# Kernel optimization log

Measured on AMD Instinct MI355X. Metric: run time of the kernel, lower is better.

## Reference

```python
import jax, jax.numpy as jnp
import numpy as np

N_NODES = 40000
N_EDGES = 640000
D = 128
D_OUT = 128


def setup_inputs() -> dict:
    key = jax.random.key(0)
    k1, k2, k3, k4, k5 = jax.random.split(key, 5)
    x = jax.random.normal(k1, (N_NODES, D), dtype=jnp.float32)
    edge_index = jax.random.randint(k2, (2, N_EDGES), 0, N_NODES, dtype=jnp.int64)
    edge_weight = jax.random.uniform(k3, (N_EDGES,), dtype=jnp.float32)
    W = jax.random.normal(k4, (D_OUT, 2 * D), dtype=jnp.float32) / np.sqrt(2 * D)
    b = jax.random.normal(k5, (D_OUT,), dtype=jnp.float32) * 0.01
    return {"x": x, "edge_index": edge_index, "edge_weight": edge_weight, "W": W, "b": b}


def reference(x, edge_index, edge_weight, W, b):
    src, dst = edge_index[0], edge_index[1]
    n_dst = x.shape[0]
    # gather source features per edge: [E, D]
    msgs = x[src]
    # per-destination weight sums (degree-normalization denominator)
    w_sum = jax.ops.segment_sum(edge_weight, dst, num_segments=n_dst)
    w_norm = edge_weight / jnp.clip(w_sum[dst], 1e-8, None)
    # weighted scatter-add aggregation: [N, D]
    agg = jax.ops.segment_sum(w_norm[:, None] * msgs, dst, num_segments=n_dst)
    # concat self + aggregated neighbors, project
    h = jnp.concatenate([x, agg], axis=-1)
    return h @ W.T + b
```

## Files before the change

### kernel.cpp

```cpp
#include <hip/hip_runtime.h>

constexpr int NN = 40000;
constexpr int NE = 640000;
constexpr int NBKT = 625;

typedef __attribute__((ext_vector_type(8))) short short8;
typedef __attribute__((ext_vector_type(4))) float f32x4;

__device__ __forceinline__ unsigned short rneb(float f) {
    unsigned u = __float_as_uint(f);
    u = (u + 0x7FFFu + ((u >> 16) & 1u)) >> 16;
    return (unsigned short)u;
}
__device__ __forceinline__ float b2f(unsigned short s) {
    return __uint_as_float(((unsigned)s) << 16);
}

__global__ void zero_k(int* __restrict__ g) {
    int t = threadIdx.x;
    if (t < NBKT) g[t] = 0;
}

__global__ __launch_bounds__(256) void cvtx_k(const float* __restrict__ x,
                                              unsigned short* __restrict__ xb) {
    int g = blockIdx.x * 256 + threadIdx.x;
    float4 v = reinterpret_cast<const float4*>(x)[g];
    ushort4 o = { rneb(v.x), rneb(v.y), rneb(v.z), rneb(v.w) };
    reinterpret_cast<ushort4*>(xb)[g] = o;
}

__global__ void cvtw_k(const float* __restrict__ W, unsigned short* __restrict__ Wb) {
    int g = blockIdx.x * 256 + threadIdx.x;
    if (g >= 128 * 64) return;
    float4 v = reinterpret_cast<const float4*>(W)[g];
    ushort4 o = { rneb(v.x), rneb(v.y), rneb(v.z), rneb(v.w) };
    reinterpret_cast<ushort4*>(Wb)[g] = o;
}

__global__ __launch_bounds__(1024) void ccount_k(const int* __restrict__ dst,
                                                 int* __restrict__ gcnt) {
    __shared__ int cnt[NBKT];
    int t = threadIdx.x;
    if (t < NBKT) cnt[t] = 0;
    __syncthreads();
    int eb = blockIdx.x * 5000;
    for (int i = t; i < 5000; i += 1024)
        atomicAdd(&cnt[dst[eb + i] >> 6], 1);
    __syncthreads();
    if (t < NBKT && cnt[t]) atomicAdd(&gcnt[t], cnt[t]);
}

__global__ __launch_bounds__(1024) void cscan_k(const int* __restrict__ gcnt,
                                                int* __restrict__ bptr,
                                                int* __restrict__ cursor) {
    __shared__ int sc[1024];
    int t = threadIdx.x;
    int c = (t < NBKT) ? gcnt[t] : 0;
    sc[t] = c;
    __syncthreads();
    for (int o = 1; o < 1024; o <<= 1) {
        int u = (t >= o) ? sc[t - o] : 0;
        __syncthreads();
        sc[t] += u;
        __syncthreads();
    }
    if (t < NBKT) {
        int excl = sc[t] - c;
        bptr[t]   = excl;
        cursor[t] = excl;
    }
    if (t == 0) bptr[NBKT] = NE;
}

__global__ __launch_bounds__(1024) void cscatter_k(const int* __restrict__ dst,
                                                   const int* __restrict__ src,
                                                   const float* __restrict__ ew,
                                                   int* __restrict__ cursor,
                                                   unsigned* __restrict__ rec,
                                                   unsigned char* __restrict__ dloc) {
    __shared__ int cnt[NBKT];
    __shared__ int base[NBKT];
    int t = threadIdx.x;
    if (t < NBKT) cnt[t] = 0;
    __syncthreads();
    int eb = blockIdx.x * 5000;
    for (int i = t; i < 5000; i += 1024)
        atomicAdd(&cnt[dst[eb + i] >> 6], 1);
    __syncthreads();
    if (t < NBKT) {
        base[t] = atomicAdd(&cursor[t], cnt[t]);
        cnt[t]  = 0;
    }
    __syncthreads();
    for (int i = t; i < 5000; i += 1024) {
        int d   = dst[eb + i];
        int bkt = d >> 6;
        int slot = atomicAdd(&cnt[bkt], 1);
        int p = base[bkt] + slot;
        unsigned short wh = __builtin_bit_cast(unsigned short, (_Float16)ew[eb + i]);
        rec[p]  = (unsigned)src[eb + i] | ((unsigned)wh << 16);
        dloc[p] = (unsigned char)(d & 63);
    }
}

__global__ __launch_bounds__(1024) void agg3_k(const unsigned* __restrict__ rec,
                                               const unsigned char* __restrict__ dloc,
                                               const int* __restrict__ bptr,
                                               const unsigned short* __restrict__ xb,
                                               float* __restrict__ out) {
    constexpr int CAP = 2048;
    __shared__ unsigned grec[CAP];
    __shared__ int cnt[64];
    __shared__ int cur[64];
    __shared__ int pL[65];
    int bkt = blockIdx.x, t = threadIdx.x;
    int beg = bptr[bkt], end = bptr[bkt + 1];
    int grp = t >> 4, fl = t & 15;
    float acc[8] = {0.f, 0.f, 0.f, 0.f, 0.f, 0.f, 0.f, 0.f};
    float wsv = 0.f;

    for (int cb = beg; cb < end; cb += CAP) {
        int m = end - cb; if (m > CAP) m = CAP;
        if (t < 64) cnt[t] = 0;
        __syncthreads();
        unsigned r0 = 0, r1 = 0; int d0 = -1, d1 = -1;
        if (t < m)        { r0 = rec[cb + t];        d0 = dloc[cb + t];        atomicAdd(&cnt[d0], 1); }
        if (t + 1024 < m) { r1 = rec[cb + t + 1024]; d1 = dloc[cb + t + 1024]; atomicAdd(&cnt[d1], 1); }
        __syncthreads();
        if (t < 64) {
            int v = cnt[t], s = v;
            #pragma unroll
            for (int o = 1; o < 64; o <<= 1) {
                int u = __shfl_up(s, o);
                if (t >= o) s += u;
            }
            pL[t]  = s - v;
            cur[t] = s - v;
            if (t == 63) pL[64] = s;
        }
        __syncthreads();
        if (d0 >= 0) { int p = atomicAdd(&cur[d0], 1); grec[p] = r0; }
        if (d1 >= 0) { int p = atomicAdd(&cur[d1], 1); grec[p] = r1; }
        __syncthreads();
        int gb = pL[grp], ge = pL[grp + 1];
        for (int e = gb; e < ge; ++e) {
            unsigned r = grec[e];
            int s = r & 0xFFFF;
            float w = (float)__builtin_bit_cast(_Float16, (unsigned short)(r >> 16));
            short8 v = *reinterpret_cast<const short8*>(xb + (size_t)s * 128 + fl * 8);
            wsv += w;
            #pragma unroll
            for (int i = 0; i < 8; ++i) acc[i] += w * b2f((unsigned short)v[i]);
        }
        __syncthreads();
    }

    int n = bkt * 64 + grp;
    float inv = 1.f / fmaxf(wsv, 1e-8f);
    float4 o0 = { acc[0] * inv, acc[1] * inv, acc[2] * inv, acc[3] * inv };
    float4 o1 = { acc[4] * inv, acc[5] * inv, acc[6] * inv, acc[7] * inv };
    float4* op = reinterpret_cast<float4*>(out + (size_t)n * 128 + fl * 8);
    op[0] = o0;
    op[1] = o1;
}

__global__ __launch_bounds__(256) void gemm_mfma_k(const unsigned short* __restrict__ xb,
                                                   const unsigned short* __restrict__ Wb,
                                                   const float* __restrict__ bias_p,
                                                   float* out) {
    int w = threadIdx.x >> 6, l = threadIdx.x & 63;
    int l15 = l & 15, lg = l >> 4;
    int rb = blockIdx.x * 128 + w * 32;

    f32x4 acc[2][8];
    #pragma unroll
    for (int i = 0; i < 2; ++i)
        #pragma unroll
        for (int c = 0; c < 8; ++c) acc[i][c] = (f32x4)0.f;

    float bias[8];
    #pragma unroll
    for (int c = 0; c < 8; ++c) bias[c] = bias_p[c * 16 + l15];

    int r0 = rb + l15;      if (r0 > NN - 1) r0 = NN - 1;
    int r1 = rb + 16 + l15; if (r1 > NN - 1) r1 = NN - 1;

    #pragma unroll
    for (int step = 0; step < 8; ++step) {
        int kg = step * 32 + lg * 8;
        short8 a0, a1;
        if (step < 4) {
            a0 = *reinterpret_cast<const short8*>(xb + (size_t)r0 * 128 + kg);
            a1 = *reinterpret_cast<const short8*>(xb + (size_t)r1 * 128 + kg);
        } else {
            const float* p0 = out + (size_t)r0 * 128 + (kg - 128);
            const float* p1 = out + (size_t)r1 * 128 + (kg - 128);
            float4 u0 = *reinterpret_cast<const float4*>(p0);
            float4 u1 = *reinterpret_cast<const float4*>(p0 + 4);
            float4 v0 = *reinterpret_cast<const float4*>(p1);
            float4 v1 = *reinterpret_cast<const float4*>(p1 + 4);
            a0 = short8{ (short)rneb(u0.x), (short)rneb(u0.y), (short)rneb(u0.z), (short)rneb(u0.w),
                         (short)rneb(u1.x), (short)rneb(u1.y), (short)rneb(u1.z), (short)rneb(u1.w) };
            a1 = short8{ (short)rneb(v0.x), (short)rneb(v0.y), (short)rneb(v0.z), (short)rneb(v0.w),
                         (short)rneb(v1.x), (short)rneb(v1.y), (short)rneb(v1.z), (short)rneb(v1.w) };
        }
        #pragma unroll
        for (int c = 0; c < 8; ++c) {
            short8 bf = *reinterpret_cast<const short8*>(Wb + (size_t)(c * 16 + l15) * 256 + kg);
            acc[0][c] = __builtin_amdgcn_mfma_f32_16x16x32_bf16(a0, bf, acc[0][c], 0, 0, 0);
            acc[1][c] = __builtin_amdgcn_mfma_f32_16x16x32_bf16(a1, bf, acc[1][c], 0, 0, 0);
        }
    }

    #pragma unroll
    for (int i = 0; i < 2; ++i) {
        int rbase = rb + i * 16 + lg * 4;
        #pragma unroll
        for (int c = 0; c < 8; ++c) {
            #pragma unroll
            for (int r = 0; r < 4; ++r) {
                int row = rbase + r;
                if (row < NN)
                    out[(size_t)row * 128 + c * 16 + l15] = acc[i][c][r] + bias[c];
            }
        }
    }
}


__global__ void wsum_k(const int* __restrict__ dst, const float* __restrict__ ew,
                       float* __restrict__ wsum) {
    int e = blockIdx.x * 256 + threadIdx.x;
    if (e < NE) atomicAdd(&wsum[dst[e]], ew[e]);
}

__global__ void zerof_k(float* __restrict__ p, int n4) {
    int g = blockIdx.x * 256 + threadIdx.x;
    if (g < n4) reinterpret_cast<float4*>(p)[g] = make_float4(0.f, 0.f, 0.f, 0.f);
}

__global__ void scatter_k(const int* __restrict__ src, const int* __restrict__ dst,
                          const float* __restrict__ ew, const float* __restrict__ wsum,
                          const float* __restrict__ x, float* __restrict__ agg) {
    int tid = blockIdx.x * 256 + threadIdx.x;
    int e = tid >> 5;
    int p = tid & 31;
    if (e >= NE) return;
    int s = src[e], dn = dst[e];
    float wn = ew[e] / fmaxf(wsum[dn], 1e-8f);
    float4 v = *reinterpret_cast<const float4*>(x + (size_t)s * 128 + p * 4);
    float* o = agg + (size_t)dn * 128 + p * 4;
    atomicAdd(o + 0, wn * v.x);
    atomicAdd(o + 1, wn * v.y);
    atomicAdd(o + 2, wn * v.z);
    atomicAdd(o + 3, wn * v.w);
}

__global__ __launch_bounds__(256) void gemm_f32_k(const float* __restrict__ x,
                                                  const float* __restrict__ agg,
                                                  const float* __restrict__ W,
                                                  const float* __restrict__ b,
                                                  float* __restrict__ out) {
    __shared__ float4 Wl[128 * 64];
    __shared__ float4 hl[16 * 64];
    int t = threadIdx.x;
    int base = blockIdx.x * 80;
    const float4* Wg = reinterpret_cast<const float4*>(W);
    #pragma unroll
    for (int i = 0; i < 32; ++i) {
        int f = t + i * 256;
        int r = f >> 6, kk = f & 63;
        Wl[r * 64 + (kk ^ (r & 7))] = Wg[f];
    }
    int jj = t & 63, wsl = t >> 6, sw = jj & 7;
    float bv[2] = { b[jj], b[jj + 64] };
    const float4* xg = reinterpret_cast<const float4*>(x);
    const float4* ag = reinterpret_cast<const float4*>(agg);
    for (int g = 0; g < 5; ++g) {
        int nbase = base + g * 16;
        __syncthreads();
        #pragma unroll
        for (int i = 0; i < 4; ++i) {
            int f = t + i * 256;
            int ln = f >> 6, kk = f & 63;
            size_t node = (size_t)(nbase + ln);
            hl[ln * 64 + kk] = (kk < 32) ? xg[node * 32 + kk] : ag[node * 32 + (kk - 32)];
        }
        __syncthreads();
        float acc[2][4];
        #pragma unroll
        for (int q = 0; q < 2; ++q)
            #pragma unroll
            for (int n = 0; n < 4; ++n) acc[q][n] = 0.f;
        #pragma unroll 4
        for (int kk = 0; kk < 64; ++kk) {
            float4 h[4];
            #pragma unroll
            for (int n = 0; n < 4; ++n) h[n] = hl[(wsl + 4 * n) * 64 + kk];
            #pragma unroll
            for (int q = 0; q < 2; ++q) {
                float4 wv = Wl[(jj + q * 64) * 64 + (kk ^ sw)];
                #pragma unroll
                for (int n = 0; n < 4; ++n)
                    acc[q][n] += wv.x * h[n].x + wv.y * h[n].y + wv.z * h[n].z + wv.w * h[n].w;
            }
        }
        #pragma unroll
        for (int q = 0; q < 2; ++q)
            #pragma unroll
            for (int n = 0; n < 4; ++n)
                out[(size_t)(nbase + wsl + 4 * n) * 128 + jj + q * 64] = acc[q][n] + bv[q];
    }
}

extern "C" void kernel_launch(void* const* d_in, const int* in_sizes, int n_in,
                              void* d_out, int out_size, void* d_ws, size_t ws_size,
                              hipStream_t stream) {
    const float* x  = (const float*)d_in[0];
    const int*   ei = (const int*)d_in[1];
    const float* ew = (const float*)d_in[2];
    const float* W  = (const float*)d_in[3];
    const float* b  = (const float*)d_in[4];
    float* out = (float*)d_out;
    const int* src = ei;
    const int* dst = ei + NE;

    const size_t off_cursor = 4096;
    const size_t off_gcnt   = 8192;
    const size_t off_Wb     = 16384;
    const size_t off_dloc   = 81920;
    const size_t off_rec    = 724992;
    const size_t off_xb     = 3284992;
    const size_t need = off_xb + (size_t)NN * 128 * 2;

    if (ws_size >= need) {
        int* bptr   = (int*)d_ws;
        int* cursor = (int*)((char*)d_ws + off_cursor);
        int* gcnt   = (int*)((char*)d_ws + off_gcnt);
        unsigned short* Wb = (unsigned short*)((char*)d_ws + off_Wb);
        unsigned char* dloc = (unsigned char*)((char*)d_ws + off_dloc);
        unsigned* rec = (unsigned*)((char*)d_ws + off_rec);
        unsigned short* xb = (unsigned short*)((char*)d_ws + off_xb);

        zero_k    <<<1, 1024, 0, stream>>>(gcnt);
        cvtx_k    <<<5000, 256, 0, stream>>>(x, xb);
        ccount_k  <<<128, 1024, 0, stream>>>(dst, gcnt);
        cscan_k   <<<1, 1024, 0, stream>>>(gcnt, bptr, cursor);
        cscatter_k<<<128, 1024, 0, stream>>>(dst, src, ew, cursor, rec, dloc);
        cvtw_k    <<<32, 256, 0, stream>>>(W, Wb);
        agg3_k    <<<NBKT, 1024, 0, stream>>>(rec, dloc, bptr, xb, out);
        gemm_mfma_k<<<(NN + 127) / 128, 256, 0, stream>>>(xb, Wb, b, out);
    } else {
        float* wsum = (float*)d_ws;
        float* agg  = out;
        zerof_k  <<<(NN / 4 + 255) / 256, 256, 0, stream>>>(wsum, NN / 4);
        zerof_k  <<<(NN * 32 + 255) / 256, 256, 0, stream>>>(agg, NN * 32);
        wsum_k   <<<(NE + 255) / 256, 256, 0, stream>>>(dst, ew, wsum);
        scatter_k<<<NE * 32 / 256, 256, 0, stream>>>(src, dst, ew, wsum, x, agg);
        gemm_f32_k<<<500, 256, 0, stream>>>(x, agg, W, b, out);
    }
}
```

Before: 97.04 us.

## Fuse aggregation with MFMA projection and merge prep kernels into one launch

Merges the x/W bf16 conversions and the bucket counting into a single prep kernel that writes per-block counts, which removes the zeroing kernel and the global atomics. Cscan now sums the per-block counts itself. The aggregation kernel keeps its normalized neighbor sums as bf16 in a swizzled shared-memory tile and runs the 64x128 output projection with MFMA in the same block. This avoids writing fp32 agg to out and reading it back in a separate GEMM, and cuts the launch count from eight to four. In exchange, 16 waves per block each compute only a small GEMM tile, re-reading W from global memory, and shared memory per block grows.

```diff
diff --git a/kernel.cpp b/kernel.cpp
--- a/kernel.cpp
+++ b/kernel.cpp
@@ -3,6 +3,7 @@
 constexpr int NN = 40000;
 constexpr int NE = 640000;
 constexpr int NBKT = 625;
+constexpr int CBLK = 128;
 
 typedef __attribute__((ext_vector_type(8))) short short8;
 typedef __attribute__((ext_vector_type(4))) float f32x4;
@@ -16,46 +17,44 @@
     return __uint_as_float(((unsigned)s) << 16);
 }
 
-__global__ void zero_k(int* __restrict__ g) {
-    int t = threadIdx.x;
-    if (t < NBKT) g[t] = 0;
-}
-
-__global__ __launch_bounds__(256) void cvtx_k(const float* __restrict__ x,
-                                              unsigned short* __restrict__ xb) {
-    int g = blockIdx.x * 256 + threadIdx.x;
-    float4 v = reinterpret_cast<const float4*>(x)[g];
-    ushort4 o = { rneb(v.x), rneb(v.y), rneb(v.z), rneb(v.w) };
-    reinterpret_cast<ushort4*>(xb)[g] = o;
-}
-
-__global__ void cvtw_k(const float* __restrict__ W, unsigned short* __restrict__ Wb) {
-    int g = blockIdx.x * 256 + threadIdx.x;
-    if (g >= 128 * 64) return;
-    float4 v = reinterpret_cast<const float4*>(W)[g];
-    ushort4 o = { rneb(v.x), rneb(v.y), rneb(v.z), rneb(v.w) };
-    reinterpret_cast<ushort4*>(Wb)[g] = o;
-}
-
-__global__ __launch_bounds__(1024) void ccount_k(const int* __restrict__ dst,
-                                                 int* __restrict__ gcnt) {
+__global__ __launch_bounds__(1024) void prep_k(const float* __restrict__ x,
+                                               unsigned short* __restrict__ xb,
+                                               const float* __restrict__ W,
+                                               unsigned short* __restrict__ Wb,
+                                               const int* __restrict__ dst,
+                                               int* __restrict__ gcnt2) {
     __shared__ int cnt[NBKT];
-    int t = threadIdx.x;
-    if (t < NBKT) cnt[t] = 0;
-    __syncthreads();
-    int eb = blockIdx.x * 5000;
-    for (int i = t; i < 5000; i += 1024)
-        atomicAdd(&cnt[dst[eb + i] >> 6], 1);
-    __syncthreads();
-    if (t < NBKT && cnt[t]) atomicAdd(&gcnt[t], cnt[t]);
-}
-
-__global__ __launch_bounds__(1024) void cscan_k(const int* __restrict__ gcnt,
+    int bid = blockIdx.x, t = threadIdx.x;
+    if (bid < 1250) {
+        int g = bid * 1024 + t;
+        float4 v = reinterpret_cast<const float4*>(x)[g];
+        ushort4 o = { rneb(v.x), rneb(v.y), rneb(v.z), rneb(v.w) };
+        reinterpret_cast<ushort4*>(xb)[g] = o;
+    } else if (bid < 1258) {
+        int g = (bid - 1250) * 1024 + t;
+        float4 v = reinterpret_cast<const float4*>(W)[g];
+        ushort4 o = { rneb(v.x), rneb(v.y), rneb(v.z), rneb(v.w) };
+        reinterpret_cast<ushort4*>(Wb)[g] = o;
+    } else {
+        int cb = bid - 1258;
+        if (t < NBKT) cnt[t] = 0;
+        __syncthreads();
+        int eb = cb * 5000;
+        for (int i = t; i < 5000; i += 1024)
+            atomicAdd(&cnt[dst[eb + i] >> 6], 1);
+        __syncthreads();
+        if (t < NBKT) gcnt2[cb * 640 + t] = cnt[t];
+    }
+}
+
+__global__ __launch_bounds__(1024) void cscan_k(const int* __restrict__ gcnt2,
                                                 int* __restrict__ bptr,
                                                 int* __restrict__ cursor) {
     __shared__ int sc[1024];
     int t = threadIdx.x;
-    int c = (t < NBKT) ? gcnt[t] : 0;
+    int c = 0;
+    if (t < NBKT)
+        for (int b = 0; b < CBLK; ++b) c += gcnt2[b * 640 + t];
     sc[t] = c;
     __syncthreads();
     for (int o = 1; o < 1024; o <<= 1) {
@@ -103,16 +102,19 @@
     }
 }
 
-__global__ __launch_bounds__(1024) void agg3_k(const unsigned* __restrict__ rec,
-                                               const unsigned char* __restrict__ dloc,
-                                               const int* __restrict__ bptr,
-                                               const unsigned short* __restrict__ xb,
-                                               float* __restrict__ out) {
+__global__ __launch_bounds__(1024) void aggemm_k(const unsigned* __restrict__ rec,
+                                                 const unsigned char* __restrict__ dloc,
+                                                 const int* __restrict__ bptr,
+                                                 const unsigned short* __restrict__ xb,
+                                                 const unsigned short* __restrict__ Wb,
+                                                 const float* __restrict__ bias_p,
+                                                 float* __restrict__ out) {
     constexpr int CAP = 2048;
     __shared__ unsigned grec[CAP];
     __shared__ int cnt[64];
     __shared__ int cur[64];
     __shared__ int pL[65];
+    __shared__ unsigned short hbl[64 * 128];
     int bkt = blockIdx.x, t = threadIdx.x;
     int beg = bptr[bkt], end = bptr[bkt + 1];
     int grp = t >> 4, fl = t & 15;
@@ -155,76 +157,48 @@
         __syncthreads();
     }
 
-    int n = bkt * 64 + grp;
-    float inv = 1.f / fmaxf(wsv, 1e-8f);
-    float4 o0 = { acc[0] * inv, acc[1] * inv, acc[2] * inv, acc[3] * inv };
-    float4 o1 = { acc[4] * inv, acc[5] * inv, acc[6] * inv, acc[7] * inv };
-    float4* op = reinterpret_cast<float4*>(out + (size_t)n * 128 + fl * 8);
-    op[0] = o0;
-    op[1] = o1;
-}
-
-__global__ __launch_bounds__(256) void gemm_mfma_k(const unsigned short* __restrict__ xb,
-                                                   const unsigned short* __restrict__ Wb,
-                                                   const float* __restrict__ bias_p,
-                                                   float* out) {
-    int w = threadIdx.x >> 6, l = threadIdx.x & 63;
+    {
+        float inv = 1.f / fmaxf(wsv, 1e-8f);
+        short8 o;
+        #pragma unroll
+        for (int i = 0; i < 8; ++i) o[i] = (short)rneb(acc[i] * inv);
+        int gs = fl ^ (grp & 7);
+        *reinterpret_cast<short8*>(&hbl[grp * 128 + gs * 8]) = o;
+    }
+    __syncthreads();
+
+    int w = t >> 6, l = t & 63;
     int l15 = l & 15, lg = l >> 4;
-    int rb = blockIdx.x * 128 + w * 32;
-
-    f32x4 acc[2][8];
-    #pragma unroll
-    for (int i = 0; i < 2; ++i)
-        #pragma unroll
-        for (int c = 0; c < 8; ++c) acc[i][c] = (f32x4)0.f;
-
-    float bias[8];
-    #pragma unroll
-    for (int c = 0; c < 8; ++c) bias[c] = bias_p[c * 16 + l15];
-
-    int r0 = rb + l15;      if (r0 > NN - 1) r0 = NN - 1;
-    int r1 = rb + 16 + l15; if (r1 > NN - 1) r1 = NN - 1;
+    int rt = w & 3, ct0 = w >> 2;
+    f32x4 acc2[2] = { (f32x4)0.f, (f32x4)0.f };
+    float bias2[2] = { bias_p[ct0 * 16 + l15], bias_p[(ct0 + 4) * 16 + l15] };
+    int arow = bkt * 64 + rt * 16 + l15;
 
     #pragma unroll
     for (int step = 0; step < 8; ++step) {
-        int kg = step * 32 + lg * 8;
-        short8 a0, a1;
+        short8 a;
         if (step < 4) {
-            a0 = *reinterpret_cast<const short8*>(xb + (size_t)r0 * 128 + kg);
-            a1 = *reinterpret_cast<const short8*>(xb + (size_t)r1 * 128 + kg);
+            a = *reinterpret_cast<const short8*>(xb + (size_t)arow * 128 + step * 32 + lg * 8);
         } else {
-            const float* p0 = out + (size_t)r0 * 128 + (kg - 128);
-            const float* p1 = out + (size_t)r1 * 128 + (kg - 128);
-            float4 u0 = *reinterpret_cast<const float4*>(p0);
-            float4 u1 = *reinterpret_cast<const float4*>(p0 + 4);
-            float4 v0 = *reinterpret_cast<const float4*>(p1);
-            float4 v1 = *reinterpret_cast<const float4*>(p1 + 4);
-            a0 = short8{ (short)rneb(u0.x), (short)rneb(u0.y), (short)rneb(u0.z), (short)rneb(u0.w),
-                         (short)rneb(u1.x), (short)rneb(u1.y), (short)rneb(u1.z), (short)rneb(u1.w) };
-            a1 = short8{ (short)rneb(v0.x), (short)rneb(v0.y), (short)rneb(v0.z), (short)rneb(v0.w),
-                         (short)rneb(v1.x), (short)rneb(v1.y), (short)rneb(v1.z), (short)rneb(v1.w) };
-        }
-        #pragma unroll
-        for (int c = 0; c < 8; ++c) {
-            short8 bf = *reinterpret_cast<const short8*>(Wb + (size_t)(c * 16 + l15) * 256 + kg);
-            acc[0][c] = __builtin_amdgcn_mfma_f32_16x16x32_bf16(a0, bf, acc[0][c], 0, 0, 0);
-            acc[1][c] = __builtin_amdgcn_mfma_f32_16x16x32_bf16(a1, bf, acc[1][c], 0, 0, 0);
+            int r = rt * 16 + l15;
+            int g = (step - 4) * 4 + lg;
+            a = *reinterpret_cast<const short8*>(&hbl[r * 128 + (g ^ (r & 7)) * 8]);
+        }
+        #pragma unroll
+        for (int q = 0; q < 2; ++q) {
+            int ct = ct0 + q * 4;
+            short8 bf = *reinterpret_cast<const short8*>(Wb + (size_t)(ct * 16 + l15) * 256 + step * 32 + lg * 8);
+            acc2[q] = __builtin_amdgcn_mfma_f32_16x16x32_bf16(a, bf, acc2[q], 0, 0, 0);
         }
     }
 
     #pragma unroll
-    for (int i = 0; i < 2; ++i) {
-        int rbase = rb + i * 16 + lg * 4;
-        #pragma unroll
-        for (int c = 0; c < 8; ++c) {
-            #pragma unroll
-            for (int r = 0; r < 4; ++r) {
-                int row = rbase + r;
-                if (row < NN)
-                    out[(size_t)row * 128 + c * 16 + l15] = acc[i][c][r] + bias[c];
-            }
-        }
-    }
+    for (int q = 0; q < 2; ++q)
+        #pragma unroll
+        for (int r4 = 0; r4 < 4; ++r4) {
+            int row = bkt * 64 + rt * 16 + lg * 4 + r4;
+            out[(size_t)row * 128 + (ct0 + q * 4) * 16 + l15] = acc2[q][r4] + bias2[q];
+        }
 }
 
 
@@ -326,30 +300,26 @@
     const int* dst = ei + NE;
 
     const size_t off_cursor = 4096;
-    const size_t off_gcnt   = 8192;
-    const size_t off_Wb     = 16384;
-    const size_t off_dloc   = 81920;
-    const size_t off_rec    = 724992;
-    const size_t off_xb     = 3284992;
+    const size_t off_gcnt2  = 8192;
+    const size_t off_Wb     = 339968;
+    const size_t off_dloc   = 405504;
+    const size_t off_rec    = 1048576;
+    const size_t off_xb     = 3670016;
     const size_t need = off_xb + (size_t)NN * 128 * 2;
 
     if (ws_size >= need) {
         int* bptr   = (int*)d_ws;
         int* cursor = (int*)((char*)d_ws + off_cursor);
-        int* gcnt   = (int*)((char*)d_ws + off_gcnt);
+        int* gcnt2  = (int*)((char*)d_ws + off_gcnt2);
         unsigned short* Wb = (unsigned short*)((char*)d_ws + off_Wb);
         unsigned char* dloc = (unsigned char*)((char*)d_ws + off_dloc);
         unsigned* rec = (unsigned*)((char*)d_ws + off_rec);
         unsigned short* xb = (unsigned short*)((char*)d_ws + off_xb);
 
-        zero_k    <<<1, 1024, 0, stream>>>(gcnt);
-        cvtx_k    <<<5000, 256, 0, stream>>>(x, xb);
-        ccount_k  <<<128, 1024, 0, stream>>>(dst, gcnt);
-        cscan_k   <<<1, 1024, 0, stream>>>(gcnt, bptr, cursor);
-        cscatter_k<<<128, 1024, 0, stream>>>(dst, src, ew, cursor, rec, dloc);
-        cvtw_k    <<<32, 256, 0, stream>>>(W, Wb);
-        agg3_k    <<<NBKT, 1024, 0, stream>>>(rec, dloc, bptr, xb, out);
-        gemm_mfma_k<<<(NN + 127) / 128, 256, 0, stream>>>(xb, Wb, b, out);
+        prep_k    <<<1386, 1024, 0, stream>>>(x, xb, W, Wb, dst, gcnt2);
+        cscan_k   <<<1, 1024, 0, stream>>>(gcnt2, bptr, cursor);
+        cscatter_k<<<CBLK, 1024, 0, stream>>>(dst, src, ew, cursor, rec, dloc);
+        aggemm_k  <<<NBKT, 1024, 0, stream>>>(rec, dloc, bptr, xb, Wb, b, out);
     } else {
         float* wsum = (float*)d_ws;
         float* agg  = out;
```

After: 92.19 us. -5.0%, faster.
